# Kernel tuning notes

Hardware: AMD Instinct MI355X
Metric: run time of the kernel (lower is better)

Reference implementation:

```python
import math
import jax, jax.numpy as jnp
import numpy as np

B, T, D, H = 2, 2048, 1024, 16
HD = D // H  # 64


def _rope(x, freq_cis):
    # x: (B, T, H, HD); freq_cis: (1, T, 1, HD//2) complex
    Bx, Tx, Hx, Dx = x.shape
    xc = jax.lax.complex(x[..., 0::2], x[..., 1::2])
    xr = xc * freq_cis
    return jnp.stack([xr.real, xr.imag], axis=-1).reshape(Bx, Tx, Hx, Dx)


def setup_inputs() -> dict:
    key = jax.random.key(0)
    ks = jax.random.split(key, 10)
    x = jax.random.normal(ks[0], (B, T, D), dtype=jnp.float32)
    # causal mask, broadcast over batch and heads
    mask = jnp.tril(jnp.ones((T, T), dtype=bool))[None, None]
    # RoPE angles: theta_j = 10000^{-2j/HD}, angle[t, j] = t * theta_j
    inv_freq = 1.0 / (10000.0 ** (jnp.arange(0, HD, 2, dtype=jnp.float32) / HD))  # (HD/2,)
    freqs = (jnp.arange(T, dtype=jnp.float32)[:, None] * inv_freq[None, :])[None, :, None, :]  # (1,T,1,HD/2)
    s = 1.0 / math.sqrt(D)
    Wq = jax.random.normal(ks[1], (D, D), dtype=jnp.float32) * s
    bq = jnp.zeros((D,), dtype=jnp.float32)
    Wk = jax.random.normal(ks[2], (D, D), dtype=jnp.float32) * s
    bk = jnp.zeros((D,), dtype=jnp.float32)
    Wv = jax.random.normal(ks[3], (D, D), dtype=jnp.float32) * s
    bv = jnp.zeros((D,), dtype=jnp.float32)
    Wo = jax.random.normal(ks[4], (D, D), dtype=jnp.float32) * s
    bo = jnp.zeros((D,), dtype=jnp.float32)
    return {"x": x, "mask": mask, "freqs": freqs,
            "Wq": Wq, "bq": bq, "Wk": Wk, "bk": bk,
            "Wv": Wv, "bv": bv, "Wo": Wo, "bo": bo}


def reference(x, mask, freqs, Wq, bq, Wk, bk, Wv, bv, Wo, bo):
    Bx, Tx, Dx = x.shape
    freq_cis = jax.lax.complex(jnp.cos(freqs), jnp.sin(freqs))  # (1,T,1,HD/2)
    q = (x @ Wq + bq).reshape(Bx, Tx, H, HD)
    k = (x @ Wk + bk).reshape(Bx, Tx, H, HD)
    v = (x @ Wv + bv).reshape(Bx, Tx, H, HD)
    q = _rope(q, freq_cis)
    k = _rope(k, freq_cis)
    # (B, H, T, HD)
    q = q.transpose(0, 2, 1, 3)
    k = k.transpose(0, 2, 1, 3)
    v = v.transpose(0, 2, 1, 3)
    attn = jnp.einsum('bhqd,bhkd->bhqk', q, k) / math.sqrt(HD)
    attn = jnp.where(mask, attn, -1e9)
    probs = jax.nn.softmax(attn, axis=-1)  # dropout is identity (deterministic=True)
    out = jnp.einsum('bhqk,bhkd->bhqd', probs, v)
    out = out.transpose(0, 2, 1, 3).reshape(Bx, Tx, Dx)
    return out @ Wo + bo
```

## Files before the change

### kernel.cpp

```cpp
#include <hip/hip_runtime.h>
#include <cstdint>
#include <cstddef>

typedef __bf16 bf16x8 __attribute__((ext_vector_type(8)));
typedef float  f32x4  __attribute__((ext_vector_type(4)));

#define DEV __device__ __forceinline__

DEV unsigned short f2bf(float f) {
  union { float f; unsigned u; } x; x.f = f;
  unsigned r = x.u + 0x7fffu + ((x.u >> 16) & 1u);
  return (unsigned short)(r >> 16);
}

DEV float fexp2(float x) {
  float r;
  asm("v_exp_f32 %0, %1" : "=v"(r) : "v"(x));
  return r;
}

DEV void gl_lds16(const void* g, void* l) {
  __builtin_amdgcn_global_load_lds((const __attribute__((address_space(1))) void*)g,
                                   (__attribute__((address_space(3))) void*)l, 16, 0, 0);
}

DEV bf16x8 lds_frag(const void* base, int byteoff) {
  return *reinterpret_cast<const bf16x8*>(reinterpret_cast<const char*>(base) + byteoff);
}

DEV f32x4 MFMA(bf16x8 a, bf16x8 b, f32x4 c) {
  return __builtin_amdgcn_mfma_f32_16x16x32_bf16(a, b, c, 0, 0, 0);
}

#define KL2E 0.18033688011112042f
#define BARRIER __builtin_amdgcn_s_barrier()

__global__ __launch_bounds__(256) void k_cast_x(const float* __restrict__ x,
                                                unsigned short* __restrict__ xb) {
  int i = (blockIdx.x * 256 + threadIdx.x) * 8;
  float4 a = *(const float4*)(x + i);
  float4 b = *(const float4*)(x + i + 4);
  uint4 o;
  o.x = (unsigned)f2bf(a.x) | ((unsigned)f2bf(a.y) << 16);
  o.y = (unsigned)f2bf(a.z) | ((unsigned)f2bf(a.w) << 16);
  o.z = (unsigned)f2bf(b.x) | ((unsigned)f2bf(b.y) << 16);
  o.w = (unsigned)f2bf(b.z) | ((unsigned)f2bf(b.w) << 16);
  *reinterpret_cast<uint4*>(xb + i) = o;
}

__global__ __launch_bounds__(256) void k_trans_w(const float* __restrict__ Wq, const float* __restrict__ Wk,
                                                 const float* __restrict__ Wv, const float* __restrict__ Wo,
                                                 unsigned short* __restrict__ WT) {
  __shared__ float tile[32][33];
  int z = blockIdx.z;
  const float* W = (z == 0) ? Wq : ((z == 1) ? Wk : ((z == 2) ? Wv : Wo));
  float scl = (z == 0) ? KL2E : 1.0f;
  unsigned short* out = WT + ((size_t)z << 20);
  int x = threadIdx.x, y = threadIdx.y;
  int gx = blockIdx.x * 32 + x;
  int gy = blockIdx.y * 32;
#pragma unroll
  for (int i = 0; i < 4; ++i) tile[y + i * 8][x] = W[(size_t)(gy + y + i * 8) * 1024 + gx];
  __syncthreads();
#pragma unroll
  for (int i = 0; i < 4; ++i)
    out[(size_t)(blockIdx.x * 32 + y + i * 8) * 1024 + gy + x] = f2bf(tile[x][y + i * 8] * scl);
}

__global__ __launch_bounds__(256) void k_cs(const float* __restrict__ freqs, float* __restrict__ tab) {
  int i = blockIdx.x * 256 + threadIdx.x;
  float a = freqs[i];
  float s, c;
  sincosf(a, &s, &c);
  ((float2*)tab)[i] = make_float2(c, s);
}

__global__ __launch_bounds__(256) void k_qkv(const unsigned short* __restrict__ xb,
                                             const unsigned short* __restrict__ WT,
                                             const float* __restrict__ bq,
                                             const float* __restrict__ bk,
                                             const float* __restrict__ bv,
                                             const float* __restrict__ tab,
                                             unsigned short* __restrict__ qws,
                                             unsigned short* __restrict__ kws,
                                             unsigned short* __restrict__ vws) {
  __shared__ __align__(16) unsigned short As[2][128 * 32];
  __shared__ __align__(16) unsigned short Bs[2][128 * 32];
  int t = threadIdx.x, w = t >> 6, l = t & 63;
  int z = blockIdx.z;
  int n0 = blockIdx.x * 128, m0 = blockIdx.y * 128;
  const unsigned short* Wz = WT + ((size_t)z << 20);
  int wm = w >> 1, wn = w & 1;
  f32x4 zero4 = {0.f, 0.f, 0.f, 0.f};
  f32x4 acc[4][4];
#pragma unroll
  for (int i = 0; i < 4; ++i)
#pragma unroll
    for (int j = 0; j < 4; ++j) acc[i][j] = zero4;

  int aoff[4], boff[4];
#pragma unroll
  for (int i = 0; i < 4; ++i) {
    aoff[i] = ((wm * 64 + i * 16 + (l & 15)) * 32 + ((l >> 4) * 8)) * 2;
    boff[i] = ((wn * 64 + i * 16 + (l & 15)) * 32 + ((l >> 4) * 8)) * 2;
  }
  int r0 = t >> 2, c0 = t & 3;

#define QSTAGE(k0v, buf) do { \
    char* la = (char*)As + (buf) * 8192 + w * 1024; \
    char* lb = (char*)Bs + (buf) * 8192 + w * 1024; \
    const char* ga0 = (const char*)xb + ((size_t)(m0 + r0) * 1024 + (k0v) + c0 * 8) * 2; \
    const char* ga1 = (const char*)xb + ((size_t)(m0 + 64 + r0) * 1024 + (k0v) + c0 * 8) * 2; \
    const char* gb0 = (const char*)Wz + ((size_t)(n0 + r0) * 1024 + (k0v) + c0 * 8) * 2; \
    const char* gb1 = (const char*)Wz + ((size_t)(n0 + 64 + r0) * 1024 + (k0v) + c0 * 8) * 2; \
    gl_lds16(ga0, la); gl_lds16(ga1, la + 4096); \
    gl_lds16(gb0, lb); gl_lds16(gb1, lb + 4096); \
  } while (0)

  QSTAGE(0, 0);
  asm volatile("s_waitcnt vmcnt(0)" ::: "memory");
  BARRIER;
  for (int k0 = 0; k0 < 1024; k0 += 32) {
    int cur = (k0 >> 5) & 1;
    if (k0 + 32 < 1024) {
      QSTAGE(k0 + 32, cur ^ 1);
      asm volatile("s_waitcnt vmcnt(4)" ::: "memory");
    } else {
      asm volatile("s_waitcnt vmcnt(0)" ::: "memory");
    }
    BARRIER;
    const char* Ab = (const char*)As + cur * 8192;
    const char* Bb = (const char*)Bs + cur * 8192;
    bf16x8 af[4], bfr[4];
#pragma unroll
    for (int i = 0; i < 4; ++i) af[i] = lds_frag(Ab, aoff[i]);
#pragma unroll
    for (int i = 0; i < 4; ++i) bfr[i] = lds_frag(Bb, boff[i]);
#pragma unroll
    for (int i = 0; i < 4; ++i)
#pragma unroll
      for (int jn = 0; jn < 4; ++jn) acc[i][jn] = MFMA(af[i], bfr[jn], acc[i][jn]);
    BARRIER;
  }
#undef QSTAGE

  const float* bias = (z == 0) ? bq : ((z == 1) ? bk : bv);
  unsigned short* outp = (z == 0) ? qws : ((z == 1) ? kws : vws);
  float bscl = (z == 0) ? KL2E : 1.0f;
  bool doRope = (z < 2);
  int nb = n0 + wn * 64, mb = m0 + wm * 64;
#pragma unroll
  for (int i = 0; i < 4; ++i) {
#pragma unroll
    for (int jn = 0; jn < 4; ++jn) {
      int n = nb + jn * 16 + (l & 15);
      float bsv = bias[n] * bscl;
      int hd = n & 63;
#pragma unroll
      for (int j = 0; j < 4; ++j) {
        int m = mb + i * 16 + ((l >> 4) << 2) + j;
        float val = acc[i][jn][j] + bsv;
        if (doRope) {
          int trow = m & 2047;
          float2 cs = ((const float2*)tab)[trow * 32 + (hd >> 1)];
          float part = __shfl_xor(val, 1);
          val = (hd & 1) ? fmaf(part, cs.y, val * cs.x) : fmaf(val, cs.x, -part * cs.y);
        }
        ((__bf16*)outp)[(size_t)m * 1024 + n] = (__bf16)val;
      }
    }
  }
}

__global__ __launch_bounds__(256) void k_vtrans(const unsigned short* __restrict__ vb,
                                                unsigned short* __restrict__ vtb) {
  __shared__ unsigned short vt[64 * 72];
  int t = threadIdx.x;
  int tt = blockIdx.x, bh = blockIdx.y;
  int b = bh >> 4, h = bh & 15;
  int row = t >> 2, ch = t & 3;
  const char* src = (const char*)vb + (((size_t)(b * 2048 + tt * 64 + row) * 1024) + h * 64 + ch * 16) * 2;
  uint4 v0 = *(const uint4*)src;
  uint4 v1 = *(const uint4*)(src + 16);
  const unsigned short* e0 = (const unsigned short*)&v0;
  const unsigned short* e1 = (const unsigned short*)&v1;
#pragma unroll
  for (int i = 0; i < 8; ++i) vt[(ch * 16 + i) * 72 + row] = e0[i];
#pragma unroll
  for (int i = 0; i < 8; ++i) vt[(ch * 16 + 8 + i) * 72 + row] = e1[i];
  __syncthreads();
  int hd = t >> 2, c2 = t & 3;
  uint4 o0 = *(const uint4*)&vt[hd * 72 + c2 * 16];
  uint4 o1 = *(const uint4*)&vt[hd * 72 + c2 * 16 + 8];
  char* dst = (char*)vtb + (((size_t)(bh * 64 + hd) * 2048) + tt * 64 + c2 * 16) * 2;
  *(uint4*)dst = o0;
  *(uint4*)(dst + 16) = o1;
}

DEV void attn_strip(const bf16x8 (&qf)[2], const bf16x8 (&kc)[2][4], const bf16x8 (&vc)[2][4],
                    f32x4 (&po)[4], f32x4 &lsum, float (&m_run)[4],
                    bool diag, unsigned short* pw, int w, int l) {
  int hi = l >> 4, lo = l & 15;
  f32x4 minit = {-m_run[0], -m_run[1], -m_run[2], -m_run[3]};
  f32x4 ps[4];
#pragma unroll
  for (int bn = 0; bn < 4; ++bn) ps[bn] = minit;
  __builtin_amdgcn_s_setprio(1);
#pragma unroll
  for (int ks = 0; ks < 2; ++ks)
#pragma unroll
    for (int bn = 0; bn < 4; ++bn) ps[bn] = MFMA(qf[ks], kc[ks][bn], ps[bn]);
  __builtin_amdgcn_s_setprio(0);
  if (diag) {
#pragma unroll
    for (int bn = 0; bn < 4; ++bn) {
      int kv = bn * 16 + lo;
#pragma unroll
      for (int j = 0; j < 4; ++j) {
        int r = (hi << 2) + j;
        if (kv > w * 16 + r) ps[bn][j] = -1e30f;
      }
    }
  }
  float t0 = fmaxf(fmaxf(ps[0][0], ps[0][1]), fmaxf(ps[0][2], ps[0][3]));
  float t1 = fmaxf(fmaxf(ps[1][0], ps[1][1]), fmaxf(ps[1][2], ps[1][3]));
  float t2 = fmaxf(fmaxf(ps[2][0], ps[2][1]), fmaxf(ps[2][2], ps[2][3]));
  float t3 = fmaxf(fmaxf(ps[3][0], ps[3][1]), fmaxf(ps[3][2], ps[3][3]));
  float tm = fmaxf(fmaxf(t0, t1), fmaxf(t2, t3));
  if (__any(tm > 8.0f)) {
    float rm[4];
#pragma unroll
    for (int j = 0; j < 4; ++j)
      rm[j] = fmaxf(fmaxf(ps[0][j], ps[1][j]), fmaxf(ps[2][j], ps[3][j]));
#pragma unroll
    for (int off = 1; off < 16; off <<= 1)
#pragma unroll
      for (int j = 0; j < 4; ++j) rm[j] = fmaxf(rm[j], __shfl_xor(rm[j], off));
    float d[4], al[4];
#pragma unroll
    for (int j = 0; j < 4; ++j) {
      d[j] = fmaxf(rm[j], 0.f);
      al[j] = fexp2(-d[j]);
      m_run[j] += d[j];
    }
#pragma unroll
    for (int bn = 0; bn < 4; ++bn)
#pragma unroll
      for (int j = 0; j < 4; ++j) ps[bn][j] -= d[j];
#pragma unroll
    for (int hf = 0; hf < 4; ++hf)
#pragma unroll
      for (int j = 0; j < 4; ++j) po[hf][j] *= al[j];
#pragma unroll
    for (int j = 0; j < 4; ++j) lsum[j] *= al[j];
  }
#pragma unroll
  for (int bn = 0; bn < 4; ++bn)
#pragma unroll
    for (int j = 0; j < 4; ++j) {
      int r = (hi << 2) + j, c = bn * 16 + lo;
      ((__bf16*)pw)[r * 64 + (((c >> 3) ^ (r & 7)) << 3) + (c & 7)] = (__bf16)fexp2(ps[bn][j]);
    }
  asm volatile("" ::: "memory");
  __bf16 one = (__bf16)1.0f;
  bf16x8 ones = {one, one, one, one, one, one, one, one};
  __builtin_amdgcn_s_setprio(1);
#pragma unroll
  for (int ks = 0; ks < 2; ++ks) {
    bf16x8 pa = lds_frag(pw, lo * 128 + (((ks * 4 + hi) ^ (lo & 7)) << 4));
#pragma unroll
    for (int hf = 0; hf < 4; ++hf) po[hf] = MFMA(pa, vc[ks][hf], po[hf]);
    lsum = MFMA(pa, ones, lsum);
  }
  __builtin_amdgcn_s_setprio(0);
  asm volatile("" ::: "memory");
}

__global__ __launch_bounds__(256) void k_attn(const unsigned short* __restrict__ qb,
                                              const unsigned short* __restrict__ kb,
                                              const unsigned short* __restrict__ vtb,
                                              unsigned short* __restrict__ ab) {
  __shared__ __align__(16) unsigned short Ks[2][64 * 64];
  __shared__ __align__(16) unsigned short Vts[2][64 * 64];
  __shared__ __align__(16) unsigned short PsA[4 * 16 * 64];
  __shared__ __align__(16) unsigned short PsB[4 * 16 * 64];
  int t = threadIdx.x, w = t >> 6, l = t & 63;
  int lid = blockIdx.x;
  int xcd = lid & 7, rest = lid >> 3;
  int bh = xcd + 8 * (rest & 3);
  int pi = rest >> 2;
  int qtA = pi, qtB = 31 - pi;
  int b = bh >> 4, h = bh & 15;
  int hi = l >> 4, lo = l & 15;

  bf16x8 qfA[2], qfB[2];
  {
    int mA = b * 2048 + qtA * 64 + w * 16 + lo;
    const char* qp = (const char*)qb + ((size_t)mA * 1024 + h * 64 + hi * 8) * 2;
    qfA[0] = *(const bf16x8*)qp;
    qfA[1] = *(const bf16x8*)(qp + 64);
    int mB = b * 2048 + qtB * 64 + w * 16 + lo;
    const char* qp2 = (const char*)qb + ((size_t)mB * 1024 + h * 64 + hi * 8) * 2;
    qfB[0] = *(const bf16x8*)qp2;
    qfB[1] = *(const bf16x8*)(qp2 + 64);
  }
  f32x4 zero4 = {0.f, 0.f, 0.f, 0.f};
  f32x4 poA[4], poB[4], lsumA = zero4, lsumB = zero4;
  float mA_[4], mB_[4];
#pragma unroll
  for (int i = 0; i < 4; ++i) {
    poA[i] = zero4; poB[i] = zero4;
    mA_[i] = 0.f;  mB_[i] = 0.f;
  }
  unsigned short* pwA = PsA + w * 1024;
  unsigned short* pwB = PsB + w * 1024;
  int r0 = t >> 3, s0 = t & 7, lc0 = s0 ^ (r0 & 7);
  int r1 = 32 + r0;
  const char* kbase = (const char*)kb + ((size_t)(b * 2048) * 1024 + h * 64) * 2;
  const char* vbase = (const char*)vtb + ((size_t)bh * 64) * 2048 * 2;

#define ASTAGE(jt, buf) do { \
    char* lk = (char*)Ks + (buf) * 8192 + w * 1024; \
    char* lv = (char*)Vts + (buf) * 8192 + w * 1024; \
    const char* gk0 = kbase + ((size_t)((jt) * 64 + r0) * 1024) * 2 + lc0 * 16; \
    const char* gk1 = kbase + ((size_t)((jt) * 64 + r1) * 1024) * 2 + lc0 * 16; \
    const char* gv0 = vbase + (size_t)r0 * 4096 + (jt) * 128 + lc0 * 16; \
    const char* gv1 = vbase + (size_t)r1 * 4096 + (jt) * 128 + lc0 * 16; \
    gl_lds16(gk0, lk); gl_lds16(gk1, lk + 4096); \
    gl_lds16(gv0, lv); gl_lds16(gv1, lv + 4096); \
  } while (0)

  ASTAGE(0, 0);
  asm volatile("s_waitcnt vmcnt(0)" ::: "memory");
  BARRIER;
  for (int jt = 0; jt <= qtB; ++jt) {
    int cur = jt & 1;
    if (jt < qtB) {
      ASTAGE(jt + 1, cur ^ 1);
      asm volatile("s_waitcnt vmcnt(4)" ::: "memory");
    } else {
      asm volatile("s_waitcnt vmcnt(0)" ::: "memory");
    }
    BARRIER;
    const char* Kb = (const char*)Ks + cur * 8192;
    const char* Vb = (const char*)Vts + cur * 8192;
    bf16x8 kc[2][4], vc[2][4];
#pragma unroll
    for (int ks = 0; ks < 2; ++ks)
#pragma unroll
      for (int i = 0; i < 4; ++i) {
        int row = i * 16 + lo;
        kc[ks][i] = lds_frag(Kb, row * 128 + (((ks * 4 + hi) ^ (lo & 7)) << 4));
        vc[ks][i] = lds_frag(Vb, row * 128 + (((ks * 4 + hi) ^ (lo & 7)) << 4));
      }
    attn_strip(qfB, kc, vc, poB, lsumB, mB_, jt == qtB, pwB, w, l);
    if (jt <= qtA) attn_strip(qfA, kc, vc, poA, lsumA, mA_, jt == qtA, pwA, w, l);
    BARRIER;
  }
#undef ASTAGE

#pragma unroll
  for (int s = 0; s < 2; ++s) {
    f32x4* po = s ? poB : poA;
    f32x4 ls = s ? lsumB : lsumA;
    int qt = s ? qtB : qtA;
    float inv[4];
#pragma unroll
    for (int j = 0; j < 4; ++j) inv[j] = 1.0f / ls[j];
#pragma unroll
    for (int hf = 0; hf < 4; ++hf)
#pragma unroll
      for (int j = 0; j < 4; ++j) {
        int r = (hi << 2) + j;
        int m = b * 2048 + qt * 64 + w * 16 + r;
        int col = h * 64 + hf * 16 + lo;
        ((__bf16*)ab)[(size_t)m * 1024 + col] = (__bf16)(po[hf][j] * inv[j]);
      }
  }
}

__global__ __launch_bounds__(256) void k_oproj(const unsigned short* __restrict__ ab,
                                               const unsigned short* __restrict__ WoT,
                                               const float* __restrict__ bo,
                                               float* __restrict__ out) {
  __shared__ __align__(16) unsigned short As[2][64 * 32];
  __shared__ __align__(16) unsigned short Bs[2][128 * 32];
  int t = threadIdx.x, w = t >> 6, l = t & 63;
  int n0 = blockIdx.x * 128, m0 = blockIdx.y * 64;
  int wm = w >> 1, wn = w & 1;
  f32x4 zero4 = {0.f, 0.f, 0.f, 0.f};
  f32x4 acc[2][4];
#pragma unroll
  for (int i = 0; i < 2; ++i)
#pragma unroll
    for (int j = 0; j < 4; ++j) acc[i][j] = zero4;
  int aoff[2], boff[4];
#pragma unroll
  for (int i = 0; i < 2; ++i)
    aoff[i] = ((wm * 32 + i * 16 + (l & 15)) * 32 + ((l >> 4) * 8)) * 2;
#pragma unroll
  for (int i = 0; i < 4; ++i)
    boff[i] = ((wn * 64 + i * 16 + (l & 15)) * 32 + ((l >> 4) * 8)) * 2;
  int ra = t >> 2, ca = t & 3;

#define OSTAGE(k0v, buf) do { \
    char* la = (char*)As + (buf) * 4096; \
    char* lb = (char*)Bs + (buf) * 8192; \
    const char* ga = (const char*)ab + ((size_t)(m0 + ra) * 1024 + (k0v) + ca * 8) * 2; \
    const char* gb0 = (const char*)WoT + ((size_t)(n0 + ra) * 1024 + (k0v) + ca * 8) * 2; \
    const char* gb1 = (const char*)WoT + ((size_t)(n0 + 64 + ra) * 1024 + (k0v) + ca * 8) * 2; \
    gl_lds16(ga, la + t * 16); \
    gl_lds16(gb0, lb + t * 16); \
    gl_lds16(gb1, lb + 4096 + t * 16); \
  } while (0)

  OSTAGE(0, 0);
  asm volatile("s_waitcnt vmcnt(0)" ::: "memory");
  BARRIER;
  for (int k0 = 0; k0 < 1024; k0 += 32) {
    int cur = (k0 >> 5) & 1;
    if (k0 + 32 < 1024) {
      OSTAGE(k0 + 32, cur ^ 1);
      asm volatile("s_waitcnt vmcnt(3)" ::: "memory");
    } else {
      asm volatile("s_waitcnt vmcnt(0)" ::: "memory");
    }
    BARRIER;
    const char* Ab = (const char*)As + cur * 4096;
    const char* Bb = (const char*)Bs + cur * 8192;
    bf16x8 af[2], bfr[4];
#pragma unroll
    for (int i = 0; i < 2; ++i) af[i] = lds_frag(Ab, aoff[i]);
#pragma unroll
    for (int i = 0; i < 4; ++i) bfr[i] = lds_frag(Bb, boff[i]);
#pragma unroll
    for (int i = 0; i < 2; ++i)
#pragma unroll
      for (int jn = 0; jn < 4; ++jn) acc[i][jn] = MFMA(af[i], bfr[jn], acc[i][jn]);
    BARRIER;
  }
#undef OSTAGE

  int nb = n0 + wn * 64, mb = m0 + wm * 32;
#pragma unroll
  for (int i = 0; i < 2; ++i)
#pragma unroll
    for (int jn = 0; jn < 4; ++jn) {
      int n = nb + jn * 16 + (l & 15);
      float bsv = bo[n];
#pragma unroll
      for (int j = 0; j < 4; ++j) {
        int m = mb + i * 16 + ((l >> 4) << 2) + j;
        out[(size_t)m * 1024 + n] = acc[i][jn][j] + bsv;
      }
    }
}

extern "C" void kernel_launch(void* const* d_in, const int* in_sizes, int n_in,
                              void* d_out, int out_size, void* d_ws, size_t ws_size,
                              hipStream_t stream) {
  const float* x     = (const float*)d_in[0];
  const float* freqs = (const float*)d_in[2];
  const float* Wq    = (const float*)d_in[3];
  const float* bq    = (const float*)d_in[4];
  const float* Wk    = (const float*)d_in[5];
  const float* bk    = (const float*)d_in[6];
  const float* Wv    = (const float*)d_in[7];
  const float* bv    = (const float*)d_in[8];
  const float* Wo    = (const float*)d_in[9];
  const float* bo    = (const float*)d_in[10];

  char* ws = (char*)d_ws;
  unsigned short* xb  = (unsigned short*)(ws);
  unsigned short* WT  = (unsigned short*)(ws + ((size_t)8 << 20));
  unsigned short* qb  = (unsigned short*)(ws + ((size_t)16 << 20));
  unsigned short* kb  = (unsigned short*)(ws + ((size_t)24 << 20));
  unsigned short* vb  = (unsigned short*)(ws + ((size_t)32 << 20));
  unsigned short* vtb = (unsigned short*)(ws + ((size_t)40 << 20));
  unsigned short* ab  = (unsigned short*)(ws + ((size_t)48 << 20));
  float*          tab = (float*)(ws + ((size_t)56 << 20));

  k_cast_x<<<2048, 256, 0, stream>>>(x, xb);
  k_trans_w<<<dim3(32, 32, 4), dim3(32, 8), 0, stream>>>(Wq, Wk, Wv, Wo, WT);
  k_cs<<<256, 256, 0, stream>>>(freqs, tab);
  k_qkv<<<dim3(8, 32, 3), 256, 0, stream>>>(xb, WT, bq, bk, bv, tab, qb, kb, vb);
  k_vtrans<<<dim3(32, 32), 256, 0, stream>>>(vb, vtb);
  k_attn<<<dim3(512), 256, 0, stream>>>(qb, kb, vtb, ab);
  k_oproj<<<dim3(8, 64), 256, 0, stream>>>(ab, WT + ((size_t)3 << 20), bo, (float*)d_out);
}
```

Baseline: 245.4 us.

## Transpose attention MFMAs to keep P in registers and launch one q-tile per block

The attention kernel now computes S^T = K·Q^T, so each lane holds one query row's scores. The row max then needs only two cross-lane shuffles, and the probabilities can be packed with v_cvt_pk_bf16_f32 and redistributed through register shuffles instead of an LDS round trip for P. The paired long/short q-tile scheme is dropped for one q-tile per block with twice as many blocks, scheduled longest-first. This removes LDS traffic and barrier pressure for P, but loses the K/V reuse across two q-tiles and shifts load balancing to the hardware scheduler.

```diff
diff --git a/kernel.cpp b/kernel.cpp
--- a/kernel.cpp
+++ b/kernel.cpp
@@ -16,6 +16,12 @@
 DEV float fexp2(float x) {
   float r;
   asm("v_exp_f32 %0, %1" : "=v"(r) : "v"(x));
+  return r;
+}
+
+DEV unsigned cvtpk(float lo, float hi) {
+  unsigned r;
+  asm("v_cvt_pk_bf16_f32 %0, %1, %2" : "=v"(r) : "v"(lo), "v"(hi));
   return r;
 }
 
@@ -197,127 +203,39 @@
   *(uint4*)(dst + 16) = o1;
 }
 
-DEV void attn_strip(const bf16x8 (&qf)[2], const bf16x8 (&kc)[2][4], const bf16x8 (&vc)[2][4],
-                    f32x4 (&po)[4], f32x4 &lsum, float (&m_run)[4],
-                    bool diag, unsigned short* pw, int w, int l) {
-  int hi = l >> 4, lo = l & 15;
-  f32x4 minit = {-m_run[0], -m_run[1], -m_run[2], -m_run[3]};
-  f32x4 ps[4];
-#pragma unroll
-  for (int bn = 0; bn < 4; ++bn) ps[bn] = minit;
-  __builtin_amdgcn_s_setprio(1);
-#pragma unroll
-  for (int ks = 0; ks < 2; ++ks)
-#pragma unroll
-    for (int bn = 0; bn < 4; ++bn) ps[bn] = MFMA(qf[ks], kc[ks][bn], ps[bn]);
-  __builtin_amdgcn_s_setprio(0);
-  if (diag) {
-#pragma unroll
-    for (int bn = 0; bn < 4; ++bn) {
-      int kv = bn * 16 + lo;
-#pragma unroll
-      for (int j = 0; j < 4; ++j) {
-        int r = (hi << 2) + j;
-        if (kv > w * 16 + r) ps[bn][j] = -1e30f;
-      }
-    }
-  }
-  float t0 = fmaxf(fmaxf(ps[0][0], ps[0][1]), fmaxf(ps[0][2], ps[0][3]));
-  float t1 = fmaxf(fmaxf(ps[1][0], ps[1][1]), fmaxf(ps[1][2], ps[1][3]));
-  float t2 = fmaxf(fmaxf(ps[2][0], ps[2][1]), fmaxf(ps[2][2], ps[2][3]));
-  float t3 = fmaxf(fmaxf(ps[3][0], ps[3][1]), fmaxf(ps[3][2], ps[3][3]));
-  float tm = fmaxf(fmaxf(t0, t1), fmaxf(t2, t3));
-  if (__any(tm > 8.0f)) {
-    float rm[4];
-#pragma unroll
-    for (int j = 0; j < 4; ++j)
-      rm[j] = fmaxf(fmaxf(ps[0][j], ps[1][j]), fmaxf(ps[2][j], ps[3][j]));
-#pragma unroll
-    for (int off = 1; off < 16; off <<= 1)
-#pragma unroll
-      for (int j = 0; j < 4; ++j) rm[j] = fmaxf(rm[j], __shfl_xor(rm[j], off));
-    float d[4], al[4];
-#pragma unroll
-    for (int j = 0; j < 4; ++j) {
-      d[j] = fmaxf(rm[j], 0.f);
-      al[j] = fexp2(-d[j]);
-      m_run[j] += d[j];
-    }
-#pragma unroll
-    for (int bn = 0; bn < 4; ++bn)
-#pragma unroll
-      for (int j = 0; j < 4; ++j) ps[bn][j] -= d[j];
-#pragma unroll
-    for (int hf = 0; hf < 4; ++hf)
-#pragma unroll
-      for (int j = 0; j < 4; ++j) po[hf][j] *= al[j];
-#pragma unroll
-    for (int j = 0; j < 4; ++j) lsum[j] *= al[j];
-  }
-#pragma unroll
-  for (int bn = 0; bn < 4; ++bn)
-#pragma unroll
-    for (int j = 0; j < 4; ++j) {
-      int r = (hi << 2) + j, c = bn * 16 + lo;
-      ((__bf16*)pw)[r * 64 + (((c >> 3) ^ (r & 7)) << 3) + (c & 7)] = (__bf16)fexp2(ps[bn][j]);
-    }
-  asm volatile("" ::: "memory");
-  __bf16 one = (__bf16)1.0f;
-  bf16x8 ones = {one, one, one, one, one, one, one, one};
-  __builtin_amdgcn_s_setprio(1);
-#pragma unroll
-  for (int ks = 0; ks < 2; ++ks) {
-    bf16x8 pa = lds_frag(pw, lo * 128 + (((ks * 4 + hi) ^ (lo & 7)) << 4));
-#pragma unroll
-    for (int hf = 0; hf < 4; ++hf) po[hf] = MFMA(pa, vc[ks][hf], po[hf]);
-    lsum = MFMA(pa, ones, lsum);
-  }
-  __builtin_amdgcn_s_setprio(0);
-  asm volatile("" ::: "memory");
-}
-
 __global__ __launch_bounds__(256) void k_attn(const unsigned short* __restrict__ qb,
                                               const unsigned short* __restrict__ kb,
                                               const unsigned short* __restrict__ vtb,
                                               unsigned short* __restrict__ ab) {
   __shared__ __align__(16) unsigned short Ks[2][64 * 64];
   __shared__ __align__(16) unsigned short Vts[2][64 * 64];
-  __shared__ __align__(16) unsigned short PsA[4 * 16 * 64];
-  __shared__ __align__(16) unsigned short PsB[4 * 16 * 64];
   int t = threadIdx.x, w = t >> 6, l = t & 63;
+  int lo = l & 15, hi = l >> 4;
   int lid = blockIdx.x;
-  int xcd = lid & 7, rest = lid >> 3;
-  int bh = xcd + 8 * (rest & 3);
-  int pi = rest >> 2;
-  int qtA = pi, qtB = 31 - pi;
+  int xcd = lid & 7;
+  int bh = xcd + 8 * ((lid >> 3) & 3);
+  int qt = 31 - (lid >> 5);
   int b = bh >> 4, h = bh & 15;
-  int hi = l >> 4, lo = l & 15;
-
-  bf16x8 qfA[2], qfB[2];
+
+  bf16x8 qf[2];
   {
-    int mA = b * 2048 + qtA * 64 + w * 16 + lo;
-    const char* qp = (const char*)qb + ((size_t)mA * 1024 + h * 64 + hi * 8) * 2;
-    qfA[0] = *(const bf16x8*)qp;
-    qfA[1] = *(const bf16x8*)(qp + 64);
-    int mB = b * 2048 + qtB * 64 + w * 16 + lo;
-    const char* qp2 = (const char*)qb + ((size_t)mB * 1024 + h * 64 + hi * 8) * 2;
-    qfB[0] = *(const bf16x8*)qp2;
-    qfB[1] = *(const bf16x8*)(qp2 + 64);
+    int m = b * 2048 + qt * 64 + w * 16 + lo;
+    const char* qp = (const char*)qb + ((size_t)m * 1024 + h * 64 + hi * 8) * 2;
+    qf[0] = *(const bf16x8*)qp;
+    qf[1] = *(const bf16x8*)(qp + 64);
   }
   f32x4 zero4 = {0.f, 0.f, 0.f, 0.f};
-  f32x4 poA[4], poB[4], lsumA = zero4, lsumB = zero4;
-  float mA_[4], mB_[4];
-#pragma unroll
-  for (int i = 0; i < 4; ++i) {
-    poA[i] = zero4; poB[i] = zero4;
-    mA_[i] = 0.f;  mB_[i] = 0.f;
-  }
-  unsigned short* pwA = PsA + w * 1024;
-  unsigned short* pwB = PsB + w * 1024;
+  f32x4 po[4], lsum = zero4;
+  float m_run = 0.f;
+#pragma unroll
+  for (int i = 0; i < 4; ++i) po[i] = zero4;
+
   int r0 = t >> 3, s0 = t & 7, lc0 = s0 ^ (r0 & 7);
   int r1 = 32 + r0;
   const char* kbase = (const char*)kb + ((size_t)(b * 2048) * 1024 + h * 64) * 2;
   const char* vbase = (const char*)vtb + ((size_t)bh * 64) * 2048 * 2;
+  __bf16 one = (__bf16)1.0f;
+  bf16x8 ones = {one, one, one, one, one, one, one, one};
 
 #define ASTAGE(jt, buf) do { \
     char* lk = (char*)Ks + (buf) * 8192 + w * 1024; \
@@ -333,9 +251,9 @@
   ASTAGE(0, 0);
   asm volatile("s_waitcnt vmcnt(0)" ::: "memory");
   BARRIER;
-  for (int jt = 0; jt <= qtB; ++jt) {
+  for (int jt = 0; jt <= qt; ++jt) {
     int cur = jt & 1;
-    if (jt < qtB) {
+    if (jt < qt) {
       ASTAGE(jt + 1, cur ^ 1);
       asm volatile("s_waitcnt vmcnt(4)" ::: "memory");
     } else {
@@ -344,38 +262,93 @@
     BARRIER;
     const char* Kb = (const char*)Ks + cur * 8192;
     const char* Vb = (const char*)Vts + cur * 8192;
-    bf16x8 kc[2][4], vc[2][4];
+
+    f32x4 ps[4];
+#pragma unroll
+    for (int bn = 0; bn < 4; ++bn) ps[bn] = (f32x4){-m_run, -m_run, -m_run, -m_run};
+    __builtin_amdgcn_s_setprio(1);
 #pragma unroll
     for (int ks = 0; ks < 2; ++ks)
 #pragma unroll
-      for (int i = 0; i < 4; ++i) {
-        int row = i * 16 + lo;
-        kc[ks][i] = lds_frag(Kb, row * 128 + (((ks * 4 + hi) ^ (lo & 7)) << 4));
-        vc[ks][i] = lds_frag(Vb, row * 128 + (((ks * 4 + hi) ^ (lo & 7)) << 4));
+      for (int bn = 0; bn < 4; ++bn) {
+        bf16x8 kcf = lds_frag(Kb, (bn * 16 + lo) * 128 + (((ks * 4 + hi) ^ (lo & 7)) << 4));
+        ps[bn] = MFMA(kcf, qf[ks], ps[bn]);
       }
-    attn_strip(qfB, kc, vc, poB, lsumB, mB_, jt == qtB, pwB, w, l);
-    if (jt <= qtA) attn_strip(qfA, kc, vc, poA, lsumA, mA_, jt == qtA, pwA, w, l);
+    __builtin_amdgcn_s_setprio(0);
+    if (jt == qt) {
+      int qrow = w * 16 + lo;
+#pragma unroll
+      for (int bn = 0; bn < 4; ++bn)
+#pragma unroll
+        for (int j = 0; j < 4; ++j)
+          if (bn * 16 + hi * 4 + j > qrow) ps[bn][j] = -1e30f;
+    }
+    float tm = ps[0][0];
+#pragma unroll
+    for (int bn = 0; bn < 4; ++bn)
+#pragma unroll
+      for (int j = 0; j < 4; ++j) tm = fmaxf(tm, ps[bn][j]);
+    if (__any(tm > 8.0f)) {
+      float rm = fmaxf(tm, __shfl_xor(tm, 16));
+      rm = fmaxf(rm, __shfl_xor(rm, 32));
+      float d = fmaxf(rm, 0.f);
+      float al = fexp2(-d);
+      m_run += d;
+#pragma unroll
+      for (int bn = 0; bn < 4; ++bn)
+#pragma unroll
+        for (int j = 0; j < 4; ++j) ps[bn][j] -= d;
+#pragma unroll
+      for (int hf = 0; hf < 4; ++hf)
+#pragma unroll
+        for (int j = 0; j < 4; ++j) po[hf][j] *= al;
+#pragma unroll
+      for (int j = 0; j < 4; ++j) lsum[j] *= al;
+    }
+    unsigned p2[4][2];
+#pragma unroll
+    for (int bn = 0; bn < 4; ++bn) {
+      p2[bn][0] = cvtpk(fexp2(ps[bn][0]), fexp2(ps[bn][1]));
+      p2[bn][1] = cvtpk(fexp2(ps[bn][2]), fexp2(ps[bn][3]));
+    }
+    int srcA = lo + 32 * (hi & 1);
+    int srcB = srcA + 16;
+    __builtin_amdgcn_s_setprio(1);
+#pragma unroll
+    for (int ks = 0; ks < 2; ++ks) {
+      unsigned a0 = __shfl(p2[2 * ks][0], srcA), a1 = __shfl(p2[2 * ks][1], srcA);
+      unsigned a2 = __shfl(p2[2 * ks][0], srcB), a3 = __shfl(p2[2 * ks][1], srcB);
+      unsigned b0 = __shfl(p2[2 * ks + 1][0], srcA), b1 = __shfl(p2[2 * ks + 1][1], srcA);
+      unsigned b2 = __shfl(p2[2 * ks + 1][0], srcB), b3 = __shfl(p2[2 * ks + 1][1], srcB);
+      uint4 wv;
+      wv.x = (hi < 2) ? a0 : b0;
+      wv.y = (hi < 2) ? a1 : b1;
+      wv.z = (hi < 2) ? a2 : b2;
+      wv.w = (hi < 2) ? a3 : b3;
+      bf16x8 pb;
+      __builtin_memcpy(&pb, &wv, 16);
+#pragma unroll
+      for (int hf = 0; hf < 4; ++hf) {
+        bf16x8 vcf = lds_frag(Vb, (hf * 16 + lo) * 128 + (((ks * 4 + hi) ^ (lo & 7)) << 4));
+        po[hf] = MFMA(vcf, pb, po[hf]);
+      }
+      lsum = MFMA(ones, pb, lsum);
+    }
+    __builtin_amdgcn_s_setprio(0);
     BARRIER;
   }
 #undef ASTAGE
 
-#pragma unroll
-  for (int s = 0; s < 2; ++s) {
-    f32x4* po = s ? poB : poA;
-    f32x4 ls = s ? lsumB : lsumA;
-    int qt = s ? qtB : qtA;
-    float inv[4];
-#pragma unroll
-    for (int j = 0; j < 4; ++j) inv[j] = 1.0f / ls[j];
-#pragma unroll
-    for (int hf = 0; hf < 4; ++hf)
-#pragma unroll
-      for (int j = 0; j < 4; ++j) {
-        int r = (hi << 2) + j;
-        int m = b * 2048 + qt * 64 + w * 16 + r;
-        int col = h * 64 + hf * 16 + lo;
-        ((__bf16*)ab)[(size_t)m * 1024 + col] = (__bf16)(po[hf][j] * inv[j]);
-      }
+  float inv = 1.0f / lsum[0];
+  int m = b * 2048 + qt * 64 + w * 16 + lo;
+#pragma unroll
+  for (int hf = 0; hf < 4; ++hf) {
+    ushort4 pk;
+    pk.x = f2bf(po[hf][0] * inv);
+    pk.y = f2bf(po[hf][1] * inv);
+    pk.z = f2bf(po[hf][2] * inv);
+    pk.w = f2bf(po[hf][3] * inv);
+    *(ushort4*)&ab[(size_t)m * 1024 + h * 64 + hf * 16 + hi * 4] = pk;
   }
 }
 
@@ -485,6 +458,6 @@
   k_cs<<<256, 256, 0, stream>>>(freqs, tab);
   k_qkv<<<dim3(8, 32, 3), 256, 0, stream>>>(xb, WT, bq, bk, bv, tab, qb, kb, vb);
   k_vtrans<<<dim3(32, 32), 256, 0, stream>>>(vb, vtb);
-  k_attn<<<dim3(512), 256, 0, stream>>>(qb, kb, vtb, ab);
+  k_attn<<<dim3(1024), 256, 0, stream>>>(qb, kb, vtb, ab);
   k_oproj<<<dim3(8, 64), 256, 0, stream>>>(ab, WT + ((size_t)3 << 20), bo, (float*)d_out);
 }
```

Result: faster. 222.4 us (-9.4%).
